# Kernel optimization log

Hardware: AMD Instinct MI355X
Metric: run time of the kernel (lower is better)

## Reference

```python
import jax, jax.numpy as jnp
import numpy as np

N, E = 10000, 320000
C_IN, C_OUT = 256, 128
EPS = 1e-5


def _p(key, shape, scale=0.02):
    return (jax.random.normal(key, shape, dtype=jnp.float32) * scale)


def setup_inputs() -> dict:
    key = jax.random.key(0)
    ks = jax.random.split(key, 16)
    inp = {
        "x": jax.random.normal(ks[0], (N, C_IN), dtype=jnp.float32),
        "edge_index": jax.random.randint(ks[1], (2, E), 0, N, dtype=jnp.int64),
        # GCNConv weights (stored [in, out] so forward is x @ W)
        "W1": _p(ks[2], (C_IN, C_OUT)), "b1": jnp.zeros((C_OUT,), jnp.float32),
        "W2": _p(ks[3], (C_OUT, C_OUT)), "b2": jnp.zeros((C_OUT,), jnp.float32),
        # LayerNorms
        "ln1_g": jnp.ones((C_OUT,), jnp.float32), "ln1_b": jnp.zeros((C_OUT,), jnp.float32),
        "ln2_g": jnp.ones((C_OUT,), jnp.float32), "ln2_b": jnp.zeros((C_OUT,), jnp.float32),
        # Attention QKV
        "Wq": _p(ks[4], (C_OUT, C_OUT)), "bq": jnp.zeros((C_OUT,), jnp.float32),
        "Wk": _p(ks[5], (C_OUT, C_OUT)), "bk": jnp.zeros((C_OUT,), jnp.float32),
        "Wv": _p(ks[6], (C_OUT, C_OUT)), "bv": jnp.zeros((C_OUT,), jnp.float32),
        # shortcut Linear (in_channels != out_channels)
        "Ws": _p(ks[7], (C_IN, C_OUT)), "bs": jnp.zeros((C_OUT,), jnp.float32),
    }
    return inp


def _gcn_conv(x, W, b, src, dst, n_nodes):
    # PyG GCNConv: h = x W; add self loops; sym-normalized scatter aggregation.
    h = x @ W  # [N, out]
    loop = jnp.arange(n_nodes, dtype=src.dtype)
    s = jnp.concatenate([src, loop])
    d = jnp.concatenate([dst, loop])
    deg = jax.ops.segment_sum(jnp.ones_like(d, dtype=h.dtype), d, num_segments=n_nodes)
    dis = jnp.where(deg > 0, jax.lax.rsqrt(deg), 0.0)  # deg^-1/2
    norm = dis[s] * dis[d]  # [E+N]
    agg = jax.ops.segment_sum(h[s] * norm[:, None], d, num_segments=n_nodes)
    return agg + b


def _layer_norm(x, g, b):
    mu = jnp.mean(x, axis=-1, keepdims=True)
    var = jnp.var(x, axis=-1, keepdims=True)
    return (x - mu) * jax.lax.rsqrt(var + EPS) * g + b


def reference(x, edge_index, W1, b1, W2, b2, ln1_g, ln1_b, ln2_g, ln2_b,
              Wq, bq, Wk, bk, Wv, bv, Ws, bs):
    src, dst = edge_index[0], edge_index[1]
    n = x.shape[0]
    identity = x @ Ws + bs
    out = _gcn_conv(x, W1, b1, src, dst, n)
    out = jax.nn.silu(_layer_norm(out, ln1_g, ln1_b))  # dropout = identity (eval)
    out = _gcn_conv(out, W2, b2, src, dst, n)
    out = _layer_norm(out, ln2_g, ln2_b)
    # dense self-attention over all nodes
    q = out @ Wq + bq
    k = out @ Wk + bk
    v = out @ Wv + bv
    scale = np.sqrt(out.shape[-1]).astype(np.float32)
    attn = jax.nn.softmax(q @ k.T / scale, axis=-1)  # [N, N]
    out = attn @ v + out
    return jax.nn.silu(out + identity)
```

## Files before the change

kernel.cpp:

```cpp
#include <hip/hip_runtime.h>
#include <hip/hip_bf16.h>

typedef unsigned short u16;
typedef unsigned int u32;
typedef __bf16 bf16x8 __attribute__((ext_vector_type(8)));
typedef float f32x4 __attribute__((ext_vector_type(4)));

#define MFMA16(a, b, c) __builtin_amdgcn_mfma_f32_16x16x32_bf16(a, b, c, 0, 0, 0)

static __device__ __forceinline__ u16 f2b(float f) {
  u32 u = __float_as_uint(f);
  return (u16)((u + 0x7FFFu + ((u >> 16) & 1u)) >> 16);
}
static __device__ __forceinline__ float blo(u32 u) { return __uint_as_float(u << 16); }
static __device__ __forceinline__ float bhi(u32 u) { return __uint_as_float(u & 0xffff0000u); }

static __device__ __forceinline__ void async_copy16(void* lds, const void* gp) {
  __builtin_amdgcn_global_load_lds(
      (const __attribute__((address_space(1))) unsigned int*)gp,
      (__attribute__((address_space(3))) unsigned int*)lds, 16, 0, 0);
}

__global__ void degi_kernel(const int* __restrict__ dst, int* __restrict__ degi, int E) {
  int e = blockIdx.x * 256 + threadIdx.x;
  if (e < E) atomicAdd(&degi[dst[e]], 1);
}

__global__ void dis_start_kernel(const int* __restrict__ degi, float* __restrict__ d,
                                 int* __restrict__ startb, int* __restrict__ counter, int N) {
  int i = blockIdx.x * 256 + threadIdx.x;
  int lane = threadIdx.x & 63;
  int dg = (i < N) ? degi[i] : 0;
  if (i < N) d[i] = rsqrtf((float)dg + 1.0f);
  int x = dg;
#pragma unroll
  for (int ofs = 1; ofs < 64; ofs <<= 1) {
    int y = __shfl_up(x, ofs, 64);
    if (lane >= ofs) x += y;
  }
  int waveTotal = __shfl(x, 63, 64);
  int base = 0;
  if (lane == 63) base = atomicAdd(counter, waveTotal);
  base = __shfl(base, 63, 64);
  if (i < N) startb[i] = base + x - dg;
}

__global__ void fill_kernel(const int* __restrict__ src, const int* __restrict__ dst,
                            const int* __restrict__ startb, int* __restrict__ cursor,
                            int* __restrict__ adj, int E) {
  int e = blockIdx.x * 256 + threadIdx.x;
  if (e < E) {
    int d = dst[e];
    int p = atomicAdd(&cursor[d], 1);
    adj[startb[d] + p] = src[e];
  }
}

__global__ void cast_all_kernel(const float* __restrict__ x, u16* __restrict__ xb, int n4,
                                const float* __restrict__ W1, const float* __restrict__ Ws,
                                const float* __restrict__ W2, const float* __restrict__ Wq,
                                const float* __restrict__ Wk, const float* __restrict__ Wv,
                                u16* __restrict__ out) {
  int t = blockIdx.x * 256 + threadIdx.x;
  if (t < n4) {
    float4 v = *(const float4*)&x[t * 4];
    ushort4 o;
    o.x = f2b(v.x); o.y = f2b(v.y); o.z = f2b(v.z); o.w = f2b(v.w);
    *(ushort4*)&xb[t * 4] = o;
    return;
  }
  int u = t - n4;
  if (u >= 131072) return;
  const float* src; int K, base, loc;
  if (u < 65536) {
    if (u < 32768) { src = W1; base = 0; } else { src = Ws; base = 32768; }
    loc = u - base; K = 256;
  } else {
    int seg = (u - 65536) >> 14;
    src = (seg == 0) ? W2 : (seg == 1) ? Wq : (seg == 2) ? Wk : Wv;
    base = 65536 + seg * 16384; loc = u & 16383; K = 128;
  }
  int k = loc >> 7, c = loc & 127;
  out[base + c * K + k] = f2b(src[loc]);
}

__global__ __launch_bounds__(64) void bgemm_dual(
    const u16* __restrict__ A, const u16* __restrict__ Wa, const u16* __restrict__ Wb,
    const float* __restrict__ bsb, u16* __restrict__ outa, float* __restrict__ outb, int M)
{
  int lane = threadIdx.x;
  int col = lane & 15, quad = lane >> 4;
  int row0 = blockIdx.x * 16;
  int cb = blockIdx.y * 64;
  int ar = row0 + col; if (ar > M - 1) ar = M - 1;
  const u16* ap = A + (size_t)ar * 256 + quad * 8;
  f32x4 Oa[4], Ob[4];
#pragma unroll
  for (int i = 0; i < 4; i++) {
    Oa[i][0] = 0.f; Oa[i][1] = 0.f; Oa[i][2] = 0.f; Oa[i][3] = 0.f;
    Ob[i] = Oa[i];
  }
#pragma unroll
  for (int k0 = 0; k0 < 256; k0 += 32) {
    bf16x8 aA = *(const bf16x8*)(ap + k0);
#pragma unroll
    for (int nb = 0; nb < 4; nb++) {
      size_t wofs = (size_t)(cb + nb * 16 + col) * 256 + k0 + quad * 8;
      Oa[nb] = MFMA16(aA, *(const bf16x8*)(Wa + wofs), Oa[nb]);
      Ob[nb] = MFMA16(aA, *(const bf16x8*)(Wb + wofs), Ob[nb]);
    }
  }
#pragma unroll
  for (int nb = 0; nb < 4; nb++) {
    int ch = cb + nb * 16 + col;
    float bv = bsb[ch];
#pragma unroll
    for (int r = 0; r < 4; r++) {
      int row = row0 + quad * 4 + r;
      if (row >= M) continue;
      outa[(size_t)row * 128 + ch] = f2b(Oa[nb][r]);
      outb[(size_t)row * 128 + ch] = Ob[nb][r] + bv;
    }
  }
}

__global__ __launch_bounds__(64) void bgemm_single(
    const u16* __restrict__ A, const u16* __restrict__ Wt, u16* __restrict__ outa, int M)
{
  int lane = threadIdx.x;
  int col = lane & 15, quad = lane >> 4;
  int row0 = blockIdx.x * 16;
  int cb = blockIdx.y * 64;
  int ar = row0 + col; if (ar > M - 1) ar = M - 1;
  const u16* ap = A + (size_t)ar * 128 + quad * 8;
  f32x4 O[4];
#pragma unroll
  for (int i = 0; i < 4; i++) { O[i][0] = 0.f; O[i][1] = 0.f; O[i][2] = 0.f; O[i][3] = 0.f; }
#pragma unroll
  for (int k0 = 0; k0 < 128; k0 += 32) {
    bf16x8 aA = *(const bf16x8*)(ap + k0);
#pragma unroll
    for (int nb = 0; nb < 4; nb++) {
      O[nb] = MFMA16(aA, *(const bf16x8*)(Wt + (size_t)(cb + nb * 16 + col) * 128 + k0 + quad * 8), O[nb]);
    }
  }
#pragma unroll
  for (int nb = 0; nb < 4; nb++) {
    int ch = cb + nb * 16 + col;
#pragma unroll
    for (int r = 0; r < 4; r++) {
      int row = row0 + quad * 4 + r;
      if (row >= M) continue;
      outa[(size_t)row * 128 + ch] = f2b(O[nb][r]);
    }
  }
}

__global__ __launch_bounds__(64) void bgemm_qkv(
    const u16* __restrict__ A, const u16* __restrict__ Wqt, const u16* __restrict__ Wkt,
    const u16* __restrict__ Wvt, const float* __restrict__ bq, const float* __restrict__ bk,
    const float* __restrict__ bv, u16* __restrict__ q_out, u16* __restrict__ k_out,
    u16* __restrict__ v_out, int M, int NP, float qscale)
{
  int lane = threadIdx.x;
  int col = lane & 15, quad = lane >> 4;
  int row0 = blockIdx.x * 16;
  int cb = blockIdx.y * 64;
  int ar = row0 + col; if (ar > M - 1) ar = M - 1;
  const u16* ap = A + (size_t)ar * 128 + quad * 8;
  f32x4 Oq[4], Ok[4], Ov[4];
#pragma unroll
  for (int i = 0; i < 4; i++) {
    Oq[i][0] = 0.f; Oq[i][1] = 0.f; Oq[i][2] = 0.f; Oq[i][3] = 0.f;
    Ok[i] = Oq[i]; Ov[i] = Oq[i];
  }
#pragma unroll
  for (int k0 = 0; k0 < 128; k0 += 32) {
    bf16x8 aA = *(const bf16x8*)(ap + k0);
#pragma unroll
    for (int nb = 0; nb < 4; nb++) {
      size_t wofs = (size_t)(cb + nb * 16 + col) * 128 + k0 + quad * 8;
      Oq[nb] = MFMA16(aA, *(const bf16x8*)(Wqt + wofs), Oq[nb]);
      Ok[nb] = MFMA16(aA, *(const bf16x8*)(Wkt + wofs), Ok[nb]);
      Ov[nb] = MFMA16(aA, *(const bf16x8*)(Wvt + wofs), Ov[nb]);
    }
  }
#pragma unroll
  for (int nb = 0; nb < 4; nb++) {
    int ch = cb + nb * 16 + col;
    float bqv = bq[ch], bkv = bk[ch], bvv = bv[ch];
#pragma unroll
    for (int r = 0; r < 4; r++) {
      int row = row0 + quad * 4 + r;
      if (row >= M) continue;
      q_out[(size_t)row * 128 + ch] = f2b((Oq[nb][r] + bqv) * qscale);
      k_out[(size_t)row * 128 + ch] = f2b(Ok[nb][r] + bkv);
      v_out[(size_t)ch * NP + row] = f2b(Ov[nb][r] + bvv);
    }
  }
}

__global__ __launch_bounds__(256) void gather_ln(
    const u16* __restrict__ h, const float* __restrict__ dis,
    const int* __restrict__ adj, const int* __restrict__ startb, const int* __restrict__ degi,
    const float* __restrict__ bias, const float* __restrict__ g, const float* __restrict__ beta,
    float* __restrict__ out, u16* __restrict__ outb, int N, int do_silu)
{
  int row = blockIdx.x * 4 + (threadIdx.x >> 6);
  int lane = threadIdx.x & 63;
  if (row >= N) return;
  int st = startb[row], dg = degi[row];
  int c2 = lane * 2;
  float v0 = 0.f, v1 = 0.f;
  for (int base = 0; base < dg; base += 64) {
    int nb = min(64, dg - base);
    int myadj = 0; float mydis = 0.f;
    if (lane < nb) { myadj = adj[st + base + lane]; mydis = dis[myadj]; }
    int jj = 0;
    for (; jj + 8 <= nb; jj += 8) {
      int s0 = __shfl(myadj, jj),     s1 = __shfl(myadj, jj + 1);
      int s2 = __shfl(myadj, jj + 2), s3 = __shfl(myadj, jj + 3);
      int s4 = __shfl(myadj, jj + 4), s5 = __shfl(myadj, jj + 5);
      int s6 = __shfl(myadj, jj + 6), s7 = __shfl(myadj, jj + 7);
      float w0 = __shfl(mydis, jj),     w1 = __shfl(mydis, jj + 1);
      float w2 = __shfl(mydis, jj + 2), w3 = __shfl(mydis, jj + 3);
      float w4 = __shfl(mydis, jj + 4), w5 = __shfl(mydis, jj + 5);
      float w6 = __shfl(mydis, jj + 6), w7 = __shfl(mydis, jj + 7);
      u32 a0 = *(const u32*)&h[(size_t)s0 * 128 + c2];
      u32 a1 = *(const u32*)&h[(size_t)s1 * 128 + c2];
      u32 a2 = *(const u32*)&h[(size_t)s2 * 128 + c2];
      u32 a3 = *(const u32*)&h[(size_t)s3 * 128 + c2];
      u32 a4 = *(const u32*)&h[(size_t)s4 * 128 + c2];
      u32 a5 = *(const u32*)&h[(size_t)s5 * 128 + c2];
      u32 a6 = *(const u32*)&h[(size_t)s6 * 128 + c2];
      u32 a7 = *(const u32*)&h[(size_t)s7 * 128 + c2];
      v0 += w0 * blo(a0); v1 += w0 * bhi(a0);
      v0 += w1 * blo(a1); v1 += w1 * bhi(a1);
      v0 += w2 * blo(a2); v1 += w2 * bhi(a2);
      v0 += w3 * blo(a3); v1 += w3 * bhi(a3);
      v0 += w4 * blo(a4); v1 += w4 * bhi(a4);
      v0 += w5 * blo(a5); v1 += w5 * bhi(a5);
      v0 += w6 * blo(a6); v1 += w6 * bhi(a6);
      v0 += w7 * blo(a7); v1 += w7 * bhi(a7);
    }
    for (; jj < nb; jj++) {
      int s = __shfl(myadj, jj);
      float wv = __shfl(mydis, jj);
      u32 a = *(const u32*)&h[(size_t)s * 128 + c2];
      v0 += wv * blo(a); v1 += wv * bhi(a);
    }
  }
  float dd = dis[row];
  u32 aself = *(const u32*)&h[(size_t)row * 128 + c2];
  v0 = (v0 + dd * blo(aself)) * dd + bias[c2];
  v1 = (v1 + dd * bhi(aself)) * dd + bias[c2 + 1];
  float s = v0 + v1;
#pragma unroll
  for (int d = 32; d > 0; d >>= 1) s += __shfl_xor(s, d, 64);
  float mu = s * (1.0f / 128.0f);
  float d0 = v0 - mu, d1 = v1 - mu;
  float q = d0 * d0 + d1 * d1;
#pragma unroll
  for (int d = 32; d > 0; d >>= 1) q += __shfl_xor(q, d, 64);
  float rstd = rsqrtf(q * (1.0f / 128.0f) + 1e-5f);
  float o0 = d0 * rstd * g[c2]     + beta[c2];
  float o1 = d1 * rstd * g[c2 + 1] + beta[c2 + 1];
  if (do_silu) {
    o0 = o0 / (1.f + __expf(-o0));
    o1 = o1 / (1.f + __expf(-o1));
  }
  size_t base = (size_t)row * 128;
  *(float2*)&out[base + c2] = make_float2(o0, o1);
  u32 pk = (u32)f2b(o0) | ((u32)f2b(o1) << 16);
  *(u32*)&outb[base + c2] = pk;
}

__global__ __launch_bounds__(256, 3) void flash_part(
    const u16* __restrict__ qb, const u16* __restrict__ kb, const u16* __restrict__ vt,
    u16* __restrict__ Opart, float* __restrict__ lpart,
    int N, int NP, int CHUNK)
{
  __shared__ __align__(16) u16 Kl[2][32 * 128];
  __shared__ __align__(16) u16 Vl[2][128 * 32];
  __shared__ __align__(16) u16 Pl[4][32][40];
  int tid = threadIdx.x;
  int w = tid >> 6, lane = tid & 63;
  int col = lane & 15, quad = lane >> 4;
  int h8 = col & 7;
  int ks = blockIdx.y;
  int kstart = ks * CHUNK;
  int qbase = blockIdx.x * 128 + w * 32;

  bf16x8 aQ[2][4];
#pragma unroll
  for (int rg = 0; rg < 2; rg++) {
    int qr = qbase + rg * 16 + col; if (qr > N - 1) qr = N - 1;
    const u16* qp = qb + (size_t)qr * 128 + quad * 8;
    aQ[rg][0] = *(const bf16x8*)(qp);
    aQ[rg][1] = *(const bf16x8*)(qp + 32);
    aQ[rg][2] = *(const bf16x8*)(qp + 64);
    aQ[rg][3] = *(const bf16x8*)(qp + 96);
  }

  f32x4 O[2][8];
#pragma unroll
  for (int rg = 0; rg < 2; rg++)
#pragma unroll
    for (int i = 0; i < 8; i++) { O[rg][i][0] = 0.f; O[rg][i][1] = 0.f; O[rg][i][2] = 0.f; O[rg][i][3] = 0.f; }
  float lr[2][4] = {{0.f, 0.f, 0.f, 0.f}, {0.f, 0.f, 0.f, 0.f}};

  int l16 = lane >> 4, c16 = lane & 15;
  int vch = lane >> 2, vc4 = lane & 3;

  auto stage = [&](int buf, int k0) {
#pragma unroll
    for (int i = 0; i < 2; i++) {
      int rl = w * 8 + i * 4 + l16;
      int cg = c16 ^ (rl & 7);
      async_copy16(&Kl[buf][(w * 8 + i * 4) * 128], kb + (size_t)(k0 + rl) * 128 + cg * 8);
    }
#pragma unroll
    for (int i = 0; i < 2; i++) {
      int ch = w * 32 + i * 16 + vch;
      int cg = vc4 ^ ((ch >> 1) & 3);
      async_copy16(&Vl[buf][(w * 32 + i * 16) * 32], vt + (size_t)ch * NP + k0 + cg * 8);
    }
  };

  int KT = (min(CHUNK, NP - kstart)) >> 5;
  stage(0, kstart);

  for (int kt = 0; kt < KT; kt++) {
    int buf = kt & 1;
    int k0 = kstart + (kt << 5);
    asm volatile("s_waitcnt vmcnt(0)\n\ts_barrier" ::: "memory");
    if (kt + 1 < KT) stage(buf ^ 1, k0 + 32);

    const u16* Kb = &Kl[buf][0];
    const u16* Vb = &Vl[buf][0];
    bool edge = (k0 + 32 > N);
#pragma unroll
    for (int g = 0; g < 2; g++) {
      const u16* kr = Kb + (g * 16 + col) * 128;
      bf16x8 kf0 = *(const bf16x8*)(kr + (((0 + quad) ^ h8) << 3));
      bf16x8 kf1 = *(const bf16x8*)(kr + (((4 + quad) ^ h8) << 3));
      bf16x8 kf2 = *(const bf16x8*)(kr + (((8 + quad) ^ h8) << 3));
      bf16x8 kf3 = *(const bf16x8*)(kr + (((12 + quad) ^ h8) << 3));
      f32x4 s0; s0[0] = 0.f; s0[1] = 0.f; s0[2] = 0.f; s0[3] = 0.f;
      f32x4 s1 = s0;
      s0 = MFMA16(aQ[0][0], kf0, s0); s1 = MFMA16(aQ[1][0], kf0, s1);
      s0 = MFMA16(aQ[0][1], kf1, s0); s1 = MFMA16(aQ[1][1], kf1, s1);
      s0 = MFMA16(aQ[0][2], kf2, s0); s1 = MFMA16(aQ[1][2], kf2, s1);
      s0 = MFMA16(aQ[0][3], kf3, s0); s1 = MFMA16(aQ[1][3], kf3, s1);
      if (edge && (k0 + g * 16 + col >= N)) {
        s0[0] = -1e30f; s0[1] = -1e30f; s0[2] = -1e30f; s0[3] = -1e30f;
        s1 = s0;
      }
#pragma unroll
      for (int r = 0; r < 4; r++) {
        float p0 = exp2f(s0[r]);
        float p1 = exp2f(s1[r]);
        lr[0][r] += p0;
        lr[1][r] += p1;
        Pl[w][quad * 4 + r][g * 16 + col]      = (u16)(__float_as_uint(p0) >> 16);
        Pl[w][16 + quad * 4 + r][g * 16 + col] = (u16)(__float_as_uint(p1) >> 16);
      }
    }
    asm volatile("s_waitcnt lgkmcnt(0)" ::: "memory");
    bf16x8 aP0 = *(const bf16x8*)&Pl[w][col][quad * 8];
    bf16x8 aP1 = *(const bf16x8*)&Pl[w][16 + col][quad * 8];
#pragma unroll
    for (int nb = 0; nb < 8; nb++) {
      int ch = nb * 16 + col;
      const u16* vr = Vb + ch * 32;
      bf16x8 vf = *(const bf16x8*)(vr + ((quad ^ ((ch >> 1) & 3)) << 3));
      O[0][nb] = MFMA16(aP0, vf, O[0][nb]);
      O[1][nb] = MFMA16(aP1, vf, O[1][nb]);
    }
  }

#pragma unroll
  for (int d = 1; d < 16; d <<= 1) {
#pragma unroll
    for (int rg = 0; rg < 2; rg++)
#pragma unroll
      for (int r = 0; r < 4; r++) lr[rg][r] += __shfl_xor(lr[rg][r], d, 64);
  }

#pragma unroll
  for (int rg = 0; rg < 2; rg++) {
#pragma unroll
    for (int nb = 0; nb < 8; nb++) {
      int ch = nb * 16 + col;
#pragma unroll
      for (int r = 0; r < 4; r++) {
        int row = qbase + rg * 16 + quad * 4 + r;
        if (row < N)
          Opart[((size_t)ks * NP + row) * 128 + ch] = f2b(O[rg][nb][r]);
      }
    }
  }
  if (col == 0) {
#pragma unroll
    for (int rg = 0; rg < 2; rg++)
#pragma unroll
      for (int r = 0; r < 4; r++) {
        int row = qbase + rg * 16 + quad * 4 + r;
        if (row < N) lpart[(size_t)ks * NP + row] = lr[rg][r];
      }
  }
}

__global__ __launch_bounds__(256) void attn_combine(
    const u16* __restrict__ Opart, const float* __restrict__ lpart,
    const float* __restrict__ out2, const float* __restrict__ ident, float* __restrict__ out,
    int N, int NP, int S)
{
  int row = blockIdx.x * 4 + (threadIdx.x >> 6);
  int c2 = (threadIdx.x & 63) * 2;
  if (row >= N) return;
  float num0 = 0.f, num1 = 0.f, den = 0.f;
  for (int u = 0; u < S; u++) {
    u32 b = *(const u32*)&Opart[((size_t)u * NP + row) * 128 + c2];
    num0 += blo(b); num1 += bhi(b);
    den += lpart[(size_t)u * NP + row];
  }
  size_t idx = (size_t)row * 128 + c2;
  float rinv = 1.0f / den;
  float2 o2 = *(const float2*)&out2[idx];
  float2 id = *(const float2*)&ident[idx];
  float v0 = num0 * rinv + o2.x + id.x;
  float v1 = num1 * rinv + o2.y + id.y;
  v0 = v0 / (1.f + __expf(-v0));
  v1 = v1 / (1.f + __expf(-v1));
  *(float2*)&out[idx] = make_float2(v0, v1);
}

extern "C" void kernel_launch(void* const* d_in, const int* in_sizes, int n_in,
                              void* d_out, int out_size, void* d_ws, size_t ws_size,
                              hipStream_t stream) {
  const float* x   = (const float*)d_in[0];
  const int*   ei  = (const int*)d_in[1];
  const float* W1  = (const float*)d_in[2];
  const float* b1  = (const float*)d_in[3];
  const float* W2  = (const float*)d_in[4];
  const float* b2  = (const float*)d_in[5];
  const float* g1  = (const float*)d_in[6];
  const float* be1 = (const float*)d_in[7];
  const float* g2  = (const float*)d_in[8];
  const float* be2 = (const float*)d_in[9];
  const float* Wq  = (const float*)d_in[10];
  const float* bq  = (const float*)d_in[11];
  const float* Wk  = (const float*)d_in[12];
  const float* bk  = (const float*)d_in[13];
  const float* Wv  = (const float*)d_in[14];
  const float* bv  = (const float*)d_in[15];
  const float* Wsw = (const float*)d_in[16];
  const float* bs  = (const float*)d_in[17];

  const int CIN = 256, C = 128;
  int N = in_sizes[0] / CIN;
  int E = in_sizes[1] / 2;
  int NP = (N + 63) & ~63;
  const int* src = ei;
  const int* dstp = ei + E;

  const int S = 8;
  int tiles = NP / 64;
  int CHUNK = ((tiles + S - 1) / S) * 64;

  char* w = (char*)d_ws;
  size_t off = 0;
  auto alloc = [&](size_t bytes) -> void* {
    void* p = w + off;
    off = (off + bytes + 255) & ~(size_t)255;
    return p;
  };
  int*   degi   = (int*)alloc((size_t)N * 4);
  int*   cursor = (int*)alloc((size_t)N * 4);
  int*   counter= (int*)alloc(256);
  size_t zlen   = off;
  float* disb   = (float*)alloc((size_t)N * 4);
  int*   startb = (int*)alloc((size_t)N * 4);
  int*   adj    = (int*)alloc((size_t)E * 4);
  u16*   h      = (u16*)alloc((size_t)N * C * 2);
  float* ident  = (float*)alloc((size_t)N * C * 4);
  float* cur    = (float*)alloc((size_t)N * C * 4);
  u16*   xb     = (u16*)alloc((size_t)N * CIN * 2);
  u16*   curb   = (u16*)alloc((size_t)N * C * 2);
  u16*   wt     = (u16*)alloc((size_t)131072 * 2);
  u16*   qbb    = (u16*)alloc((size_t)N * C * 2);
  u16*   kbb    = (u16*)alloc((size_t)NP * C * 2);
  u16*   vt     = (u16*)alloc((size_t)C * NP * 2);
  u16*   Opart  = (u16*)alloc((size_t)S * NP * C * 2);
  float* lpart  = (float*)alloc((size_t)S * NP * 4);

  u16* wt1 = wt;
  u16* wts = wt + 32768;
  u16* wt2 = wt + 65536;
  u16* wtq = wt + 81920;
  u16* wtk = wt + 98304;
  u16* wtv = wt + 114688;

  hipMemsetAsync(degi, 0, zlen, stream);

  int gE = (E + 255) / 256, gN = (N + 255) / 256;
  degi_kernel<<<gE, 256, 0, stream>>>(dstp, degi, E);
  dis_start_kernel<<<gN, 256, 0, stream>>>(degi, disb, startb, counter, N);
  fill_kernel<<<gE, 256, 0, stream>>>(src, dstp, startb, cursor, adj, E);

  int n4 = N * CIN / 4;
  int ctot = n4 + 131072;
  cast_all_kernel<<<(ctot + 255) / 256, 256, 0, stream>>>(x, xb, n4, W1, Wsw, W2, Wq, Wk, Wv, wt);

  dim3 gbg((N + 15) / 16, 2);
  bgemm_dual<<<gbg, 64, 0, stream>>>(xb, wt1, wts, bs, h, ident, N);
  gather_ln<<<(N + 3) / 4, 256, 0, stream>>>(h, disb, adj, startb, degi, b1, g1, be1, cur, curb, N, 1);
  bgemm_single<<<gbg, 64, 0, stream>>>(curb, wt2, h, N);
  gather_ln<<<(N + 3) / 4, 256, 0, stream>>>(h, disb, adj, startb, degi, b2, g2, be2, cur, curb, N, 0);

  const float qscale = 0.12753224f;
  bgemm_qkv<<<gbg, 64, 0, stream>>>(curb, wtq, wtk, wtv, bq, bk, bv, qbb, kbb, vt, N, NP, qscale);

  dim3 fg((N + 127) / 128, S);
  flash_part<<<fg, 256, 0, stream>>>(qbb, kbb, vt, Opart, lpart, N, NP, CHUNK);
  attn_combine<<<(N + 3) / 4, 256, 0, stream>>>(Opart, lpart, cur, ident,
                                                (float*)d_out, N, NP, S);
}
```

Before: 299.8 us.

## Fuse degree count into cast kernel, raise attention split, switch exp2 to expf

Merges the degree-count atomic kernel into the bf16 cast kernel to save one launch. It raises the flash-attention key split from 8 to 12 partitions so more blocks run in parallel, at the cost of a larger partial buffer and more combine work. It also replaces exp2f with __expf and changes the q scale from 1/sqrt(128)*log2(e) to plain 1/sqrt(128), which keeps the maths equivalent. Max subtraction is not visible in this loop either way.

```diff
diff --git a/kernel.cpp b/kernel.cpp
--- a/kernel.cpp
+++ b/kernel.cpp
@@ -21,55 +21,23 @@
       (__attribute__((address_space(3))) unsigned int*)lds, 16, 0, 0);
 }
 
-__global__ void degi_kernel(const int* __restrict__ dst, int* __restrict__ degi, int E) {
-  int e = blockIdx.x * 256 + threadIdx.x;
-  if (e < E) atomicAdd(&degi[dst[e]], 1);
-}
-
-__global__ void dis_start_kernel(const int* __restrict__ degi, float* __restrict__ d,
-                                 int* __restrict__ startb, int* __restrict__ counter, int N) {
-  int i = blockIdx.x * 256 + threadIdx.x;
-  int lane = threadIdx.x & 63;
-  int dg = (i < N) ? degi[i] : 0;
-  if (i < N) d[i] = rsqrtf((float)dg + 1.0f);
-  int x = dg;
-#pragma unroll
-  for (int ofs = 1; ofs < 64; ofs <<= 1) {
-    int y = __shfl_up(x, ofs, 64);
-    if (lane >= ofs) x += y;
-  }
-  int waveTotal = __shfl(x, 63, 64);
-  int base = 0;
-  if (lane == 63) base = atomicAdd(counter, waveTotal);
-  base = __shfl(base, 63, 64);
-  if (i < N) startb[i] = base + x - dg;
-}
-
-__global__ void fill_kernel(const int* __restrict__ src, const int* __restrict__ dst,
-                            const int* __restrict__ startb, int* __restrict__ cursor,
-                            int* __restrict__ adj, int E) {
-  int e = blockIdx.x * 256 + threadIdx.x;
-  if (e < E) {
-    int d = dst[e];
-    int p = atomicAdd(&cursor[d], 1);
-    adj[startb[d] + p] = src[e];
-  }
-}
-
-__global__ void cast_all_kernel(const float* __restrict__ x, u16* __restrict__ xb, int n4,
-                                const float* __restrict__ W1, const float* __restrict__ Ws,
-                                const float* __restrict__ W2, const float* __restrict__ Wq,
-                                const float* __restrict__ Wk, const float* __restrict__ Wv,
-                                u16* __restrict__ out) {
+__global__ void prep_kernel(const int* __restrict__ dst, int* __restrict__ degi, int E,
+                            const float* __restrict__ x, u16* __restrict__ xb, int n4,
+                            const float* __restrict__ W1, const float* __restrict__ Ws,
+                            const float* __restrict__ W2, const float* __restrict__ Wq,
+                            const float* __restrict__ Wk, const float* __restrict__ Wv,
+                            u16* __restrict__ wout) {
   int t = blockIdx.x * 256 + threadIdx.x;
-  if (t < n4) {
-    float4 v = *(const float4*)&x[t * 4];
+  if (t < E) { atomicAdd(&degi[dst[t]], 1); return; }
+  int t2 = t - E;
+  if (t2 < n4) {
+    float4 v = *(const float4*)&x[t2 * 4];
     ushort4 o;
     o.x = f2b(v.x); o.y = f2b(v.y); o.z = f2b(v.z); o.w = f2b(v.w);
-    *(ushort4*)&xb[t * 4] = o;
+    *(ushort4*)&xb[t2 * 4] = o;
     return;
   }
-  int u = t - n4;
+  int u = t2 - n4;
   if (u >= 131072) return;
   const float* src; int K, base, loc;
   if (u < 65536) {
@@ -81,7 +49,37 @@
     base = 65536 + seg * 16384; loc = u & 16383; K = 128;
   }
   int k = loc >> 7, c = loc & 127;
-  out[base + c * K + k] = f2b(src[loc]);
+  wout[base + c * K + k] = f2b(src[loc]);
+}
+
+__global__ void dis_start_kernel(const int* __restrict__ degi, float* __restrict__ d,
+                                 int* __restrict__ startb, int* __restrict__ counter, int N) {
+  int i = blockIdx.x * 256 + threadIdx.x;
+  int lane = threadIdx.x & 63;
+  int dg = (i < N) ? degi[i] : 0;
+  if (i < N) d[i] = rsqrtf((float)dg + 1.0f);
+  int x = dg;
+#pragma unroll
+  for (int ofs = 1; ofs < 64; ofs <<= 1) {
+    int y = __shfl_up(x, ofs, 64);
+    if (lane >= ofs) x += y;
+  }
+  int waveTotal = __shfl(x, 63, 64);
+  int base = 0;
+  if (lane == 63) base = atomicAdd(counter, waveTotal);
+  base = __shfl(base, 63, 64);
+  if (i < N) startb[i] = base + x - dg;
+}
+
+__global__ void fill_kernel(const int* __restrict__ src, const int* __restrict__ dst,
+                            const int* __restrict__ startb, int* __restrict__ cursor,
+                            int* __restrict__ adj, int E) {
+  int e = blockIdx.x * 256 + threadIdx.x;
+  if (e < E) {
+    int d = dst[e];
+    int p = atomicAdd(&cursor[d], 1);
+    adj[startb[d] + p] = src[e];
+  }
 }
 
 __global__ __launch_bounds__(64) void bgemm_dual(
@@ -358,8 +356,8 @@
       }
 #pragma unroll
       for (int r = 0; r < 4; r++) {
-        float p0 = exp2f(s0[r]);
-        float p1 = exp2f(s1[r]);
+        float p0 = __expf(s0[r]);
+        float p1 = __expf(s1[r]);
         lr[0][r] += p0;
         lr[1][r] += p1;
         Pl[w][quad * 4 + r][g * 16 + col]      = (u16)(__float_as_uint(p0) >> 16);
@@ -465,7 +463,7 @@
   const int* src = ei;
   const int* dstp = ei + E;
 
-  const int S = 8;
+  const int S = 12;
   int tiles = NP / 64;
   int CHUNK = ((tiles + S - 1) / S) * 64;
 
@@ -504,14 +502,13 @@
 
   hipMemsetAsync(degi, 0, zlen, stream);
 
-  int gE = (E + 255) / 256, gN = (N + 255) / 256;
-  degi_kernel<<<gE, 256, 0, stream>>>(dstp, degi, E);
+  int n4 = N * CIN / 4;
+  int ptot = E + n4 + 131072;
+  prep_kernel<<<(ptot + 255) / 256, 256, 0, stream>>>(dstp, degi, E, x, xb, n4,
+                                                      W1, Wsw, W2, Wq, Wk, Wv, wt);
+  int gN = (N + 255) / 256, gE = (E + 255) / 256;
   dis_start_kernel<<<gN, 256, 0, stream>>>(degi, disb, startb, counter, N);
   fill_kernel<<<gE, 256, 0, stream>>>(src, dstp, startb, cursor, adj, E);
-
-  int n4 = N * CIN / 4;
-  int ctot = n4 + 131072;
-  cast_all_kernel<<<(ctot + 255) / 256, 256, 0, stream>>>(x, xb, n4, W1, Wsw, W2, Wq, Wk, Wv, wt);
 
   dim3 gbg((N + 15) / 16, 2);
   bgemm_dual<<<gbg, 64, 0, stream>>>(xb, wt1, wts, bs, h, ident, N);
@@ -519,7 +516,7 @@
   bgemm_single<<<gbg, 64, 0, stream>>>(curb, wt2, h, N);
   gather_ln<<<(N + 3) / 4, 256, 0, stream>>>(h, disb, adj, startb, degi, b2, g2, be2, cur, curb, N, 0);
 
-  const float qscale = 0.12753224f;
+  const float qscale = 0.08838834764831845f;
   bgemm_qkv<<<gbg, 64, 0, stream>>>(curb, wtq, wtk, wtv, bq, bk, bv, qbb, kbb, vt, N, NP, qscale);
 
   dim3 fg((N + 127) / 128, S);
```

Result: no change. 295.8 us (-1.4%).
